# Kernel optimization log

Hardware: AMD Instinct MI355X
Metric: run time of the kernel (lower is better)

Reference implementation:

```python
import jax, jax.numpy as jnp
import numpy as np
import math

D_MODEL = 2048
N_HEADS = 16
HEAD_DIM = 128
ROPE_THETA = 10000.0


def apply_rope(x, pos, theta=ROPE_THETA):
    # x: [b, h, s, d], pos: [b, s] int
    d = x.shape[-1]
    inv_freq = 1.0 / (theta ** (jnp.arange(0, d, 2, dtype=jnp.float32) / d))  # [d/2]
    ang = pos.astype(jnp.float32)[:, None, :, None] * inv_freq  # [b,1,s,d/2]
    cos, sin = jnp.cos(ang), jnp.sin(ang)
    x1, x2 = x[..., 0::2], x[..., 1::2]
    out_even = x1 * cos - x2 * sin
    out_odd = x1 * sin + x2 * cos
    return jnp.stack([out_even, out_odd], axis=-1).reshape(x.shape)


def setup_inputs() -> dict:
    key = jax.random.key(0)
    ks = jax.random.split(key, 5)
    b, s = 2, 2048
    scale = 1.0 / math.sqrt(D_MODEL)
    x = jax.random.normal(ks[0], (b, s, D_MODEL), dtype=jnp.float32)
    Wq = jax.random.normal(ks[1], (D_MODEL, D_MODEL), dtype=jnp.float32) * scale
    Wk = jax.random.normal(ks[2], (D_MODEL, D_MODEL), dtype=jnp.float32) * scale
    Wv = jax.random.normal(ks[3], (D_MODEL, D_MODEL), dtype=jnp.float32) * scale
    Wo = jax.random.normal(ks[4], (D_MODEL, D_MODEL), dtype=jnp.float32) * scale
    token_positions = jnp.broadcast_to(jnp.arange(s, dtype=jnp.int32), (b, s))
    return {"x": x, "token_positions": token_positions, "Wq": Wq, "Wk": Wk, "Wv": Wv, "Wo": Wo}


def reference(x, token_positions, Wq, Wk, Wv, Wo):
    b, s, _ = x.shape
    h, d = N_HEADS, HEAD_DIM
    # QKV projections (Linear: x @ W.T), split heads: b s (h d) -> b h s d
    def proj(W):
        y = jnp.einsum('bse,fe->bsf', x, W)
        return y.reshape(b, s, h, d).transpose(0, 2, 1, 3)
    Q, K, V = proj(Wq), proj(Wk), proj(Wv)
    Q = apply_rope(Q, token_positions)
    K = apply_rope(K, token_positions)
    logits = jnp.einsum('bhqd,bhkd->bhqk', Q, K) / math.sqrt(d)
    causal = jnp.triu(jnp.ones((s, s), dtype=bool), 1)
    logits = jnp.where(causal, -jnp.inf, logits)
    attn = jax.nn.softmax(logits, axis=-1)
    ctx = jnp.einsum('bhqk,bhkd->bhqd', attn, V)
    ctx = ctx.transpose(0, 2, 1, 3).reshape(b, s, h * d)
    return jnp.einsum('bsf,ef->bse', ctx, Wo)
```

## Files before the change

kernel.cpp:

```cpp
#include <hip/hip_runtime.h>
#include <cstdint>
#include <cstddef>

typedef __bf16 bf16_t;
typedef __bf16 bf16x8 __attribute__((ext_vector_type(8)));
typedef float  f32x4  __attribute__((ext_vector_type(4)));

#define SEQ 2048
#define NH  16
#define HD  128
#define MM  4096
#define KK  2048

#define ASYNC16(g, l) __builtin_amdgcn_global_load_lds( \
    (const __attribute__((address_space(1))) void*)(g), \
    (__attribute__((address_space(3))) void*)(l), 16, 0, 0)

__global__ __launch_bounds__(256) void cast_f32_bf16(const float* __restrict__ src,
                                                     bf16_t* __restrict__ dst, int n4) {
    int i = blockIdx.x * 256 + threadIdx.x;
    if (i >= n4) return;
    float4 v = ((const float4*)src)[i];
    union { bf16_t h[4]; uint2 u; } t;
    t.h[0] = (bf16_t)v.x; t.h[1] = (bf16_t)v.y;
    t.h[2] = (bf16_t)v.z; t.h[3] = (bf16_t)v.w;
    ((uint2*)dst)[i] = t.u;
}

__global__ __launch_bounds__(256) void cast_w4(const float* __restrict__ Wq,
                                               const float* __restrict__ Wk,
                                               const float* __restrict__ Wv,
                                               const float* __restrict__ Wo,
                                               bf16_t* __restrict__ wqkv,
                                               bf16_t* __restrict__ wob) {
    int i = blockIdx.x * 256 + threadIdx.x;
    int sel = i >> 20;
    int off = i & 0xFFFFF;
    const float* src = (sel == 0) ? Wq : (sel == 1) ? Wk : (sel == 2) ? Wv : Wo;
    bf16_t* dst = (sel < 3) ? (wqkv + (size_t)sel * 4194304) : wob;
    float4 v = ((const float4*)src)[off];
    union { bf16_t h[4]; uint2 u; } t;
    t.h[0] = (bf16_t)v.x; t.h[1] = (bf16_t)v.y;
    t.h[2] = (bf16_t)v.z; t.h[3] = (bf16_t)v.w;
    ((uint2*)dst)[off] = t.u;
}

template<int MODE>
__global__ __launch_bounds__(256) void gemm_bt(const bf16_t* __restrict__ A,
                                               const bf16_t* __restrict__ B,
                                               void* __restrict__ Cout,
                                               bf16_t* __restrict__ Kout,
                                               bf16_t* __restrict__ Vout) {
    __shared__ bf16_t ldsA[8 * 512];
    __shared__ bf16_t ldsB[8 * 512];

    const int tid = threadIdx.x;
    const int w = tid >> 6, l = tid & 63;
    const int lane16 = l & 15, quad = l >> 4;
    const int tm = blockIdx.y, tn = blockIdx.x;
    const int wm = w >> 1, wn = w & 1;

    const bf16_t* pA0 = A + (size_t)(tm * 128 + (2 * w + 0) * 16 + lane16) * KK + quad * 8;
    const bf16_t* pA1 = A + (size_t)(tm * 128 + (2 * w + 1) * 16 + lane16) * KK + quad * 8;
    const bf16_t* pB0 = B + (size_t)(tn * 128 + (2 * w + 0) * 16 + lane16) * KK + quad * 8;
    const bf16_t* pB1 = B + (size_t)(tn * 128 + (2 * w + 1) * 16 + lane16) * KK + quad * 8;

    bf16_t* wA0 = &ldsA[(2 * w + 0) * 512];
    bf16_t* wA1 = &ldsA[(2 * w + 1) * 512];
    bf16_t* wB0 = &ldsB[(2 * w + 0) * 512];
    bf16_t* wB1 = &ldsB[(2 * w + 1) * 512];
    const bf16_t* rA = &ldsA[wm * 4 * 512 + l * 8];
    const bf16_t* rB = &ldsB[wn * 4 * 512 + l * 8];

    f32x4 acc[4][4];
    for (int i = 0; i < 4; i++)
        for (int j = 0; j < 4; j++) acc[i][j] = (f32x4){0.f, 0.f, 0.f, 0.f};

    for (int k0 = 0; k0 < KK; k0 += 32) {
        __syncthreads();
        ASYNC16(pA0, wA0); ASYNC16(pA1, wA1);
        ASYNC16(pB0, wB0); ASYNC16(pB1, wB1);
        pA0 += 32; pA1 += 32; pB0 += 32; pB1 += 32;
        __syncthreads();
        bf16x8 af[4], bfr[4];
        for (int i = 0; i < 4; i++) af[i]  = *(const bf16x8*)(rA + i * 512);
        for (int j = 0; j < 4; j++) bfr[j] = *(const bf16x8*)(rB + j * 512);
        for (int i = 0; i < 4; i++)
            for (int j = 0; j < 4; j++)
                acc[i][j] = __builtin_amdgcn_mfma_f32_16x16x32_bf16(af[i], bfr[j], acc[i][j], 0, 0, 0);
    }

    const int mbase = tm * 128 + wm * 64;
    const int nbase = tn * 128 + wn * 64;
    for (int i = 0; i < 4; i++) {
        for (int j = 0; j < 4; j++) {
            const int n  = nbase + j * 16 + lane16;
            const int m0 = mbase + i * 16 + quad * 4;
            if (MODE == 3) {
                const int sel = n >> 11;
                const int n2 = n & 2047;
                const int h = n2 >> 7, d = n2 & 127;
                if (sel < 2) {
                    bf16_t* dst = (sel == 0) ? (bf16_t*)Cout : Kout;
                    for (int r = 0; r < 4; r++) {
                        const int m = m0 + r, b = m >> 11, s = m & 2047;
                        dst[(((size_t)(b * NH + h) * SEQ + s) * HD) + d] = (bf16_t)acc[i][j][r];
                    }
                } else {
                    const int b = m0 >> 11, s = m0 & 2047;
                    union { bf16_t h4[4]; ushort4 u; } tv;
                    for (int r = 0; r < 4; r++) tv.h4[r] = (bf16_t)acc[i][j][r];
                    *(ushort4*)(Vout + ((size_t)(b * NH + h) * HD + d) * SEQ + s) = tv.u;
                }
            } else {
                for (int r = 0; r < 4; r++) {
                    const int m = m0 + r;
                    ((float*)Cout)[(size_t)m * 2048 + n] = acc[i][j][r];
                }
            }
        }
    }
}

__global__ __launch_bounds__(256) void rope_kernel(bf16_t* __restrict__ Q,
                                                   bf16_t* __restrict__ K,
                                                   const int* __restrict__ pos) {
    int gid = blockIdx.x * 256 + threadIdx.x;
    int i  = gid & 63;
    int s  = (gid >> 6) & 2047;
    int bh = gid >> 17;
    int b  = bh >> 4;
    float p = (float)pos[b * SEQ + s];
    float freq = exp2f(-(float)i * 0.20762050593045857f);
    float ang = p * freq;
    float sn, cs;
    sincosf(ang, &sn, &cs);
    const float scale = 0.08838834764831845f;
    size_t base = ((size_t)bh * SEQ + s) * HD + 2 * i;
    {
        float q1 = (float)Q[base], q2 = (float)Q[base + 1];
        Q[base]     = (bf16_t)((q1 * cs - q2 * sn) * scale);
        Q[base + 1] = (bf16_t)((q1 * sn + q2 * cs) * scale);
    }
    {
        float k1 = (float)K[base], k2 = (float)K[base + 1];
        K[base]     = (bf16_t)(k1 * cs - k2 * sn);
        K[base + 1] = (bf16_t)(k1 * sn + k2 * cs);
    }
}

__global__ __launch_bounds__(256) void attn_kernel(const bf16_t* __restrict__ Q,
                                                   const bf16_t* __restrict__ K,
                                                   const bf16_t* __restrict__ Vt,
                                                   bf16_t* __restrict__ ctx) {
    const int flat = blockIdx.x;
    const int bh = flat & 31;
    const int bt = flat >> 5;
    const int h = bh & 15, b = bh >> 4;
    const bf16_t* Qh = Q  + (size_t)bh * SEQ * HD;
    const bf16_t* Kh = K  + (size_t)bh * SEQ * HD;
    const bf16_t* Vh = Vt + (size_t)bh * HD * SEQ;

    const int tid = threadIdx.x;
    const int w = tid >> 6, l = tid & 63;
    const int lane16 = l & 15, quad = l >> 4;

    __shared__ bf16_t kt[2][16 * 512];
    __shared__ bf16_t vt[2][16 * 512];
    __shared__ bf16_t pbuf[4][1024];

    for (int half = 0; half < 2; half++) {
        const int qt = half ? (31 - bt) : bt;
        const int q0 = qt * 64 + w * 16;

        bf16x8 qf[4];
        {
            const bf16_t* qrow = Qh + (size_t)(q0 + lane16) * HD + quad * 8;
            for (int kc = 0; kc < 4; kc++) qf[kc] = *(const bf16x8*)(qrow + kc * 32);
        }

        f32x4 o[8];
        for (int dt = 0; dt < 8; dt++) o[dt] = (f32x4){0.f, 0.f, 0.f, 0.f};
        float m_s = -INFINITY, l_s = 0.f;

        __syncthreads();
        for (int ii = 0; ii < 4; ii++) {
            const int f = w * 4 + ii;
            const int nt = f >> 2, kc = f & 3;
            ASYNC16(Kh + (size_t)(nt * 16 + lane16) * HD + kc * 32 + quad * 8, &kt[0][f * 512]);
            const int dt = f >> 1, kk = f & 1;
            ASYNC16(Vh + (size_t)(dt * 16 + lane16) * SEQ + kk * 32 + quad * 8, &vt[0][f * 512]);
        }

        int cur = 0;
        for (int kb = 0; kb <= qt; kb++) {
            const int k0 = kb * 64;
            __syncthreads();
            if (kb < qt) {
                const int kn = k0 + 64;
                for (int ii = 0; ii < 4; ii++) {
                    const int f = w * 4 + ii;
                    const int nt = f >> 2, kc = f & 3;
                    ASYNC16(Kh + (size_t)(kn + nt * 16 + lane16) * HD + kc * 32 + quad * 8,
                            &kt[1 - cur][f * 512]);
                    const int dt = f >> 1, kk = f & 1;
                    ASYNC16(Vh + (size_t)(dt * 16 + lane16) * SEQ + kn + kk * 32 + quad * 8,
                            &vt[1 - cur][f * 512]);
                }
            }
            const bf16_t* ktc = kt[cur];
            const bf16_t* vtc = vt[cur];

            f32x4 sacc[4];
            for (int nt = 0; nt < 4; nt++) sacc[nt] = (f32x4){0.f, 0.f, 0.f, 0.f};
            for (int nt = 0; nt < 4; nt++)
                for (int kc = 0; kc < 4; kc++) {
                    bf16x8 kf = *(const bf16x8*)&ktc[(nt * 4 + kc) * 512 + l * 8];
                    sacc[nt] = __builtin_amdgcn_mfma_f32_16x16x32_bf16(kf, qf[kc], sacc[nt], 0, 0, 0);
                }
            if (kb == qt) {
                const int qg = q0 + lane16;
                for (int nt = 0; nt < 4; nt++)
                    for (int r = 0; r < 4; r++) {
                        const int kg = k0 + nt * 16 + quad * 4 + r;
                        if (kg > qg) sacc[nt][r] = -INFINITY;
                    }
            }
            float rowmax = sacc[0][0];
            for (int nt = 0; nt < 4; nt++)
                for (int r = 0; r < 4; r++) rowmax = fmaxf(rowmax, sacc[nt][r]);
            rowmax = fmaxf(rowmax, __shfl_xor(rowmax, 16, 64));
            rowmax = fmaxf(rowmax, __shfl_xor(rowmax, 32, 64));
            const float mnew = fmaxf(m_s, rowmax);
            const float a = __expf(m_s - mnew);
            m_s = mnew;
            float ssum = 0.f;
            for (int nt = 0; nt < 4; nt++) {
                union { bf16_t h4[4]; uint2 u; } pk;
                for (int r = 0; r < 4; r++) {
                    const float e = __expf(sacc[nt][r] - mnew);
                    ssum += e;
                    pk.h4[r] = (bf16_t)e;
                }
                const int addr = (nt >> 1) * 512 +
                                 (((nt & 1) * 2 + (quad >> 1)) * 16 + lane16) * 8 +
                                 (quad & 1) * 4;
                *(uint2*)&pbuf[w][addr] = pk.u;
            }
            ssum += __shfl_xor(ssum, 16, 64);
            ssum += __shfl_xor(ssum, 32, 64);
            l_s = l_s * a + ssum;

            float ar[4];
            for (int r = 0; r < 4; r++) ar[r] = __shfl(a, (quad << 2) | r, 16);
            for (int dt = 0; dt < 8; dt++)
                for (int r = 0; r < 4; r++) o[dt][r] *= ar[r];
            for (int kk = 0; kk < 2; kk++) {
                bf16x8 pf = *(const bf16x8*)&pbuf[w][kk * 512 + l * 8];
                for (int dt = 0; dt < 8; dt++) {
                    bf16x8 vf = *(const bf16x8*)&vtc[(dt * 2 + kk) * 512 + l * 8];
                    o[dt] = __builtin_amdgcn_mfma_f32_16x16x32_bf16(pf, vf, o[dt], 0, 0, 0);
                }
            }
            cur ^= 1;
        }

        float inv[4];
        for (int r = 0; r < 4; r++) inv[r] = 1.0f / __shfl(l_s, (quad << 2) | r, 16);
        for (int r = 0; r < 4; r++) {
            const int qg = q0 + quad * 4 + r;
            bf16_t* dst = ctx + ((size_t)(b * SEQ + qg)) * (NH * HD) + h * HD;
            for (int dt = 0; dt < 8; dt++)
                dst[dt * 16 + lane16] = (bf16_t)(o[dt][r] * inv[r]);
        }
        __syncthreads();
    }
}

extern "C" void kernel_launch(void* const* d_in, const int* in_sizes, int n_in,
                              void* d_out, int out_size, void* d_ws, size_t ws_size,
                              hipStream_t stream) {
    const float* x  = (const float*)d_in[0];
    const int* pos  = (const int*)d_in[1];
    const float* Wq = (const float*)d_in[2];
    const float* Wk = (const float*)d_in[3];
    const float* Wv = (const float*)d_in[4];
    const float* Wo = (const float*)d_in[5];

    char* ws = (char*)d_ws;
    bf16_t* xb   = (bf16_t*)(ws);
    bf16_t* wqkv = (bf16_t*)(ws + (16u << 20));
    bf16_t* wob  = (bf16_t*)(ws + (40u << 20));
    bf16_t* Qb   = (bf16_t*)(ws + (48u << 20));
    bf16_t* Kb   = (bf16_t*)(ws + (64u << 20));
    bf16_t* Vt   = (bf16_t*)(ws + (80u << 20));
    bf16_t* ctx  = (bf16_t*)(ws + (96u << 20));

    cast_f32_bf16<<<8192, 256, 0, stream>>>(x, xb, 2097152);
    cast_w4<<<16384, 256, 0, stream>>>(Wq, Wk, Wv, Wo, wqkv, wob);

    dim3 gq(6144 / 128, MM / 128);
    gemm_bt<3><<<gq, 256, 0, stream>>>(xb, wqkv, (void*)Qb, Kb, Vt);

    rope_kernel<<<16384, 256, 0, stream>>>(Qb, Kb, pos);

    attn_kernel<<<512, 256, 0, stream>>>(Qb, Kb, Vt, ctx);

    dim3 gg(2048 / 128, MM / 128);
    gemm_bt<1><<<gg, 256, 0, stream>>>(ctx, wob, d_out, nullptr, nullptr);
}
```

Measured before the change: 479.9 us.

## Fuse RoPE into QKV GEMM epilogue with LDS-staged coalesced stores

Removes the separate RoPE kernel by applying rotary embedding and Q scaling inside the QKV GEMM epilogue. Accumulators are staged through a shared-memory buffer so Q/K rows and transposed V rows are written as 16-byte coalesced stores instead of scattered 2-byte and 8-byte stores. The two cast kernels are merged into one launch. In exchange the epilogue adds extra barriers and shared-memory round trips, and uses fast __sinf/__cosf, which lose accuracy for large angles.

New measurement: 471.1 us. No clear change (-1.8%).

```diff
diff --git a/kernel.cpp b/kernel.cpp
--- a/kernel.cpp
+++ b/kernel.cpp
@@ -16,28 +16,25 @@
     (const __attribute__((address_space(1))) void*)(g), \
     (__attribute__((address_space(3))) void*)(l), 16, 0, 0)
 
-__global__ __launch_bounds__(256) void cast_f32_bf16(const float* __restrict__ src,
-                                                     bf16_t* __restrict__ dst, int n4) {
+__global__ __launch_bounds__(256) void cast_all(const float* __restrict__ x,
+                                                const float* __restrict__ Wq,
+                                                const float* __restrict__ Wk,
+                                                const float* __restrict__ Wv,
+                                                const float* __restrict__ Wo,
+                                                bf16_t* __restrict__ xb,
+                                                bf16_t* __restrict__ wqkv,
+                                                bf16_t* __restrict__ wob) {
     int i = blockIdx.x * 256 + threadIdx.x;
-    if (i >= n4) return;
-    float4 v = ((const float4*)src)[i];
-    union { bf16_t h[4]; uint2 u; } t;
-    t.h[0] = (bf16_t)v.x; t.h[1] = (bf16_t)v.y;
-    t.h[2] = (bf16_t)v.z; t.h[3] = (bf16_t)v.w;
-    ((uint2*)dst)[i] = t.u;
-}
-
-__global__ __launch_bounds__(256) void cast_w4(const float* __restrict__ Wq,
-                                               const float* __restrict__ Wk,
-                                               const float* __restrict__ Wv,
-                                               const float* __restrict__ Wo,
-                                               bf16_t* __restrict__ wqkv,
-                                               bf16_t* __restrict__ wob) {
-    int i = blockIdx.x * 256 + threadIdx.x;
-    int sel = i >> 20;
-    int off = i & 0xFFFFF;
-    const float* src = (sel == 0) ? Wq : (sel == 1) ? Wk : (sel == 2) ? Wv : Wo;
-    bf16_t* dst = (sel < 3) ? (wqkv + (size_t)sel * 4194304) : wob;
+    const float* src;
+    bf16_t* dst;
+    int off;
+    if (i < 2097152) { src = x; dst = xb; off = i; }
+    else {
+        int j = i - 2097152;
+        int sel = j >> 20; off = j & 0xFFFFF;
+        if (sel < 3) { src = (sel == 0) ? Wq : (sel == 1) ? Wk : Wv; dst = wqkv + (size_t)sel * 4194304; }
+        else         { src = Wo; dst = wob; }
+    }
     float4 v = ((const float4*)src)[off];
     union { bf16_t h[4]; uint2 u; } t;
     t.h[0] = (bf16_t)v.x; t.h[1] = (bf16_t)v.y;
@@ -50,9 +47,12 @@
                                                const bf16_t* __restrict__ B,
                                                void* __restrict__ Cout,
                                                bf16_t* __restrict__ Kout,
-                                               bf16_t* __restrict__ Vout) {
-    __shared__ bf16_t ldsA[8 * 512];
-    __shared__ bf16_t ldsB[8 * 512];
+                                               bf16_t* __restrict__ Vout,
+                                               const int* __restrict__ pos) {
+    __shared__ union SMem {
+        struct { bf16_t A[8 * 512]; bf16_t B[8 * 512]; } st;
+        bf16_t epi[64 * 136];
+    } sm;
 
     const int tid = threadIdx.x;
     const int w = tid >> 6, l = tid & 63;
@@ -65,12 +65,12 @@
     const bf16_t* pB0 = B + (size_t)(tn * 128 + (2 * w + 0) * 16 + lane16) * KK + quad * 8;
     const bf16_t* pB1 = B + (size_t)(tn * 128 + (2 * w + 1) * 16 + lane16) * KK + quad * 8;
 
-    bf16_t* wA0 = &ldsA[(2 * w + 0) * 512];
-    bf16_t* wA1 = &ldsA[(2 * w + 1) * 512];
-    bf16_t* wB0 = &ldsB[(2 * w + 0) * 512];
-    bf16_t* wB1 = &ldsB[(2 * w + 1) * 512];
-    const bf16_t* rA = &ldsA[wm * 4 * 512 + l * 8];
-    const bf16_t* rB = &ldsB[wn * 4 * 512 + l * 8];
+    bf16_t* wA0 = &sm.st.A[(2 * w + 0) * 512];
+    bf16_t* wA1 = &sm.st.A[(2 * w + 1) * 512];
+    bf16_t* wB0 = &sm.st.B[(2 * w + 0) * 512];
+    bf16_t* wB1 = &sm.st.B[(2 * w + 1) * 512];
+    const bf16_t* rA = &sm.st.A[wm * 4 * 512 + l * 8];
+    const bf16_t* rB = &sm.st.B[wn * 4 * 512 + l * 8];
 
     f32x4 acc[4][4];
     for (int i = 0; i < 4; i++)
@@ -90,62 +90,80 @@
                 acc[i][j] = __builtin_amdgcn_mfma_f32_16x16x32_bf16(af[i], bfr[j], acc[i][j], 0, 0, 0);
     }
 
-    const int mbase = tm * 128 + wm * 64;
-    const int nbase = tn * 128 + wn * 64;
-    for (int i = 0; i < 4; i++) {
-        for (int j = 0; j < 4; j++) {
-            const int n  = nbase + j * 16 + lane16;
-            const int m0 = mbase + i * 16 + quad * 4;
-            if (MODE == 3) {
-                const int sel = n >> 11;
-                const int n2 = n & 2047;
-                const int h = n2 >> 7, d = n2 & 127;
-                if (sel < 2) {
-                    bf16_t* dst = (sel == 0) ? (bf16_t*)Cout : Kout;
-                    for (int r = 0; r < 4; r++) {
-                        const int m = m0 + r, b = m >> 11, s = m & 2047;
-                        dst[(((size_t)(b * NH + h) * SEQ + s) * HD) + d] = (bf16_t)acc[i][j][r];
+    if (MODE == 1) {
+        const int mbase = tm * 128 + wm * 64;
+        const int nbase = tn * 128 + wn * 64;
+        for (int i = 0; i < 4; i++)
+            for (int j = 0; j < 4; j++) {
+                const int n  = nbase + j * 16 + lane16;
+                const int m0 = mbase + i * 16 + quad * 4;
+                for (int r = 0; r < 4; r++)
+                    ((float*)Cout)[(size_t)(m0 + r) * 2048 + n] = acc[i][j][r];
+            }
+        return;
+    }
+
+    const int mbase = tm * 128;
+    const int nb    = tn * 128;
+    const int sel   = nb >> 11;
+    const int hh    = (nb & 2047) >> 7;
+    const int bidx  = mbase >> 11;
+    const int g  = tid >> 4;
+    const int c8 = (tid & 15) * 8;
+
+    if (sel < 2) {
+        bf16_t* dstbase = ((sel == 0) ? (bf16_t*)Cout : Kout) +
+                          (size_t)(bidx * NH + hh) * SEQ * HD;
+        const float qs = (sel == 0) ? 0.08838834764831845f : 1.0f;
+        for (int half = 0; half < 2; half++) {
+            __syncthreads();
+            if (wm == half) {
+                for (int i = 0; i < 4; i++)
+                    for (int j = 0; j < 4; j++)
+                        for (int r = 0; r < 4; r++)
+                            sm.epi[(i * 16 + quad * 4 + r) * 136 + wn * 64 + j * 16 + lane16] =
+                                (bf16_t)acc[i][j][r];
+            }
+            __syncthreads();
+            for (int p = 0; p < 4; p++) {
+                const int rid = p * 16 + g;
+                const int s = (mbase & 2047) + half * 64 + rid;
+                bf16x8 v = *(const bf16x8*)&sm.epi[rid * 136 + c8];
+                const float pp = (float)pos[bidx * SEQ + s];
+                union { bf16_t h8[8]; uint4 u; } o;
+                for (int t = 0; t < 4; t++) {
+                    const int fi = (c8 >> 1) + t;
+                    const float freq = exp2f(-(float)fi * 0.20762050593045857f);
+                    const float ang = pp * freq;
+                    const float sn = __sinf(ang), cs = __cosf(ang);
+                    const float x1 = (float)v[2 * t], x2 = (float)v[2 * t + 1];
+                    o.h8[2 * t]     = (bf16_t)((x1 * cs - x2 * sn) * qs);
+                    o.h8[2 * t + 1] = (bf16_t)((x1 * sn + x2 * cs) * qs);
+                }
+                *(uint4*)(dstbase + (size_t)s * HD + c8) = o.u;
+            }
+        }
+    } else {
+        bf16_t* dstb = Vout + (size_t)(bidx * NH + hh) * HD * SEQ;
+        const int s0 = mbase & 2047;
+        for (int half = 0; half < 2; half++) {
+            __syncthreads();
+            if (wn == half) {
+                for (int i = 0; i < 4; i++)
+                    for (int j = 0; j < 4; j++) {
+                        union { bf16_t h4[4]; uint2 u; } pk;
+                        for (int r = 0; r < 4; r++) pk.h4[r] = (bf16_t)acc[i][j][r];
+                        *(uint2*)&sm.epi[(j * 16 + lane16) * 136 + wm * 64 + i * 16 + quad * 4] = pk.u;
                     }
-                } else {
-                    const int b = m0 >> 11, s = m0 & 2047;
-                    union { bf16_t h4[4]; ushort4 u; } tv;
-                    for (int r = 0; r < 4; r++) tv.h4[r] = (bf16_t)acc[i][j][r];
-                    *(ushort4*)(Vout + ((size_t)(b * NH + h) * HD + d) * SEQ + s) = tv.u;
-                }
-            } else {
-                for (int r = 0; r < 4; r++) {
-                    const int m = m0 + r;
-                    ((float*)Cout)[(size_t)m * 2048 + n] = acc[i][j][r];
-                }
-            }
-        }
-    }
-}
-
-__global__ __launch_bounds__(256) void rope_kernel(bf16_t* __restrict__ Q,
-                                                   bf16_t* __restrict__ K,
-                                                   const int* __restrict__ pos) {
-    int gid = blockIdx.x * 256 + threadIdx.x;
-    int i  = gid & 63;
-    int s  = (gid >> 6) & 2047;
-    int bh = gid >> 17;
-    int b  = bh >> 4;
-    float p = (float)pos[b * SEQ + s];
-    float freq = exp2f(-(float)i * 0.20762050593045857f);
-    float ang = p * freq;
-    float sn, cs;
-    sincosf(ang, &sn, &cs);
-    const float scale = 0.08838834764831845f;
-    size_t base = ((size_t)bh * SEQ + s) * HD + 2 * i;
-    {
-        float q1 = (float)Q[base], q2 = (float)Q[base + 1];
-        Q[base]     = (bf16_t)((q1 * cs - q2 * sn) * scale);
-        Q[base + 1] = (bf16_t)((q1 * sn + q2 * cs) * scale);
-    }
-    {
-        float k1 = (float)K[base], k2 = (float)K[base + 1];
-        K[base]     = (bf16_t)(k1 * cs - k2 * sn);
-        K[base + 1] = (bf16_t)(k1 * sn + k2 * cs);
+            }
+            __syncthreads();
+            for (int p = 0; p < 4; p++) {
+                const int rid = p * 16 + g;
+                const int d = half * 64 + rid;
+                bf16x8 v = *(const bf16x8*)&sm.epi[rid * 136 + c8];
+                *(uint4*)(dstb + (size_t)d * SEQ + s0 + c8) = *(const uint4*)&v;
+            }
+        }
     }
 }
 
@@ -296,16 +314,13 @@
     bf16_t* Vt   = (bf16_t*)(ws + (80u << 20));
     bf16_t* ctx  = (bf16_t*)(ws + (96u << 20));
 
-    cast_f32_bf16<<<8192, 256, 0, stream>>>(x, xb, 2097152);
-    cast_w4<<<16384, 256, 0, stream>>>(Wq, Wk, Wv, Wo, wqkv, wob);
+    cast_all<<<24576, 256, 0, stream>>>(x, Wq, Wk, Wv, Wo, xb, wqkv, wob);
 
     dim3 gq(6144 / 128, MM / 128);
-    gemm_bt<3><<<gq, 256, 0, stream>>>(xb, wqkv, (void*)Qb, Kb, Vt);
-
-    rope_kernel<<<16384, 256, 0, stream>>>(Qb, Kb, pos);
+    gemm_bt<3><<<gq, 256, 0, stream>>>(xb, wqkv, (void*)Qb, Kb, Vt, pos);
 
     attn_kernel<<<512, 256, 0, stream>>>(Qb, Kb, Vt, ctx);
 
     dim3 gg(2048 / 128, MM / 128);
-    gemm_bt<1><<<gg, 256, 0, stream>>>(ctx, wob, d_out, nullptr, nullptr);
+    gemm_bt<1><<<gg, 256, 0, stream>>>(ctx, wob, d_out, nullptr, nullptr, nullptr);
 }
```
